# Kernel optimization log

Measured on AMD Instinct MI355X. Metric: run time of the kernel, lower is better.

The kernel has to match this reference:

```python
import jax, jax.numpy as jnp
import numpy as np

BN_EPS = 1e-5


def setup_inputs() -> dict:
    key = jax.random.key(0)
    ks = jax.random.split(key, 16)
    N, E, D, H = 100000, 1200000, 64, 128
    return {
        "x": jax.random.normal(ks[0], (N, D), dtype=jnp.float32),
        "edge_index": jax.random.randint(ks[1], (2, E), 0, N, dtype=jnp.int64),
        "edge_weight": jax.random.uniform(ks[2], (E,), dtype=jnp.float32),
        "edge_features": jax.random.normal(ks[3], (E, 16), dtype=jnp.float32),
        "adj": jnp.zeros((1,), dtype=jnp.float32),
        "T": 1,
        "bn_gamma": jax.random.uniform(ks[4], (D,), dtype=jnp.float32) + 0.5,
        "bn_beta": jax.random.normal(ks[5], (D,), dtype=jnp.float32) * 0.1,
        "W_l": jax.random.normal(ks[6], (D, H), dtype=jnp.float32) / np.sqrt(D),
        "b_l": jax.random.normal(ks[7], (H,), dtype=jnp.float32) * 0.01,
        "W_r": jax.random.normal(ks[8], (D, H), dtype=jnp.float32) / np.sqrt(D),
        "W1": jax.random.normal(ks[9], (H, 16), dtype=jnp.float32) / np.sqrt(H),
        "b1": jax.random.normal(ks[10], (16,), dtype=jnp.float32) * 0.01,
        "W2": jax.random.normal(ks[11], (16, 2), dtype=jnp.float32) / 4.0,
        "b2": jax.random.normal(ks[12], (2,), dtype=jnp.float32) * 0.01,
    }


def reference(x, edge_index, edge_weight, edge_features, adj, T,
              bn_gamma, bn_beta, W_l, b_l, W_r, W1, b1, W2, b2):
    # edge_weight, edge_features, adj, T are accepted but unused, matching the
    # original module's forward.
    N = x.shape[0]
    # BatchNorm1d (training mode: batch statistics, biased variance)
    mean = jnp.mean(x, axis=0)
    var = jnp.var(x, axis=0)
    xn = (x - mean) * jax.lax.rsqrt(var + BN_EPS) * bn_gamma + bn_beta

    # SAGEConv with mean aggregation: out = lin_l(mean_{j->i} x_j) + lin_r(x_i)
    src, dst = edge_index[0], edge_index[1]
    agg = jax.ops.segment_sum(xn[src], dst, num_segments=N)  # [N, D]
    deg = jax.ops.segment_sum(jnp.ones_like(dst, dtype=xn.dtype), dst,
                              num_segments=N)
    agg = agg / jnp.maximum(deg, 1.0)[:, None]
    h = agg @ W_l + b_l + xn @ W_r  # [N, H]
    h = jax.nn.relu(h)

    # classifier head: Linear(H,16) -> ReLU -> Linear(16,2)
    out = jax.nn.relu(h @ W1 + b1) @ W2 + b2  # [N, 2]
    return out
```

## Files before the change

### kernel.cpp

```cpp
#include <hip/hip_runtime.h>

#define FEAT 64
#define HDIM 128
#define BN_EPS 1e-5f

#define BSH 7
#define NB_MAX 1024
#define SCHUNK 4096
#define SEG 4096
#define CAP 2048

#define PSOFF 1280
#define PQOFF (PSOFF + 65536)
#define WCOFF (PQOFF + 65536)
#define XNOFF (WCOFF + 8192)

typedef __attribute__((ext_vector_type(8))) short bf16x8;
typedef __attribute__((ext_vector_type(4))) float f32x4;

#define GL16(gp, lp)                                                        \
    __builtin_amdgcn_global_load_lds(                                       \
        (const __attribute__((address_space(1))) unsigned int*)(gp),        \
        (__attribute__((address_space(3))) unsigned int*)(lp), 16, 0, 0)

__device__ inline unsigned short f2bf(float f) {
    union { float f; unsigned int u; } v;
    v.f = f;
    unsigned int r = (v.u + 0x7FFFu + ((v.u >> 16) & 1u)) >> 16;
    return (unsigned short)r;
}
__device__ inline float bf2f(unsigned short b) {
    union { unsigned int u; float f; } v;
    v.u = ((unsigned int)b) << 16;
    return v.f;
}

__global__ __launch_bounds__(256) void kA(const float* __restrict__ x,
                                          float* __restrict__ ws,
                                          const float* __restrict__ Wl,
                                          const float* __restrict__ Wr,
                                          unsigned short* __restrict__ Wc,
                                          const int* __restrict__ ei,
                                          int* __restrict__ bktCnt,
                                          int* __restrict__ pairs,
                                          int N, int E, int nb, int sbin) {
    __shared__ float4 sS[4][16];
    __shared__ float4 sQ[4][16];
    __shared__ int hist[NB_MAX];
    __shared__ int base[NB_MAX];
    int blk = blockIdx.x, t = threadIdx.x;
    if (blk < sbin) {
        int chunk = blk;
        int e0 = chunk * SCHUNK;
        int e1 = min(E, e0 + SCHUNK);
        for (int b = t; b < nb; b += 256) hist[b] = 0;
        __syncthreads();
        for (int e = e0 + t; e < e1; e += 256)
            atomicAdd(&hist[((unsigned)ei[E + e]) >> BSH], 1);
        __syncthreads();
        int rot = (chunk * 131) % nb;
        for (int j = t; j < nb; j += 256) {
            int b = j + rot;
            if (b >= nb) b -= nb;
            int c = hist[b];
            base[b] = c ? atomicAdd(&bktCnt[b], c) : 0;
            hist[b] = 0;
        }
        __syncthreads();
        for (int e = e0 + t; e < e1; e += 256) {
            int src = ei[e];
            int dst = ei[E + e];
            int b = ((unsigned)dst) >> BSH;
            int off = atomicAdd(&hist[b], 1);
            int pos = base[b] + off;
            if (pos < CAP) pairs[b * CAP + pos] = (src << BSH) | (dst & 127);
        }
    } else if (blk < sbin + 1024) {
        int sblk = blk - sbin;
        int rpb = (N + 1023) >> 10;
        int colg = t & 15, rowi = t >> 4;
        int lane = t & 63, wv = t >> 6;
        const float4* x4 = (const float4*)x;
        float4 s4 = {0.f, 0.f, 0.f, 0.f}, q4 = {0.f, 0.f, 0.f, 0.f};
        int r0 = sblk * rpb;
        for (int i = rowi; i < rpb; i += 16) {
            int r = r0 + i;
            if (r < N) {
                float4 v = x4[r * 16 + colg];
                s4.x += v.x; s4.y += v.y; s4.z += v.z; s4.w += v.w;
                q4.x += v.x * v.x; q4.y += v.y * v.y;
                q4.z += v.z * v.z; q4.w += v.w * v.w;
            }
        }
#pragma unroll
        for (int mk = 16; mk <= 32; mk <<= 1) {
            s4.x += __shfl_xor(s4.x, mk); s4.y += __shfl_xor(s4.y, mk);
            s4.z += __shfl_xor(s4.z, mk); s4.w += __shfl_xor(s4.w, mk);
            q4.x += __shfl_xor(q4.x, mk); q4.y += __shfl_xor(q4.y, mk);
            q4.z += __shfl_xor(q4.z, mk); q4.w += __shfl_xor(q4.w, mk);
        }
        if (lane < 16) { sS[wv][lane] = s4; sQ[wv][lane] = q4; }
        __syncthreads();
        if (t < 16) {
            float4 a = sS[0][t], b4 = sQ[0][t];
#pragma unroll
            for (int w = 1; w < 4; w++) {
                a.x += sS[w][t].x; a.y += sS[w][t].y;
                a.z += sS[w][t].z; a.w += sS[w][t].w;
                b4.x += sQ[w][t].x; b4.y += sQ[w][t].y;
                b4.z += sQ[w][t].z; b4.w += sQ[w][t].w;
            }
            int c0 = t * 4;
            ws[PSOFF + (c0 + 0) * 1024 + sblk] = a.x;
            ws[PSOFF + (c0 + 1) * 1024 + sblk] = a.y;
            ws[PSOFF + (c0 + 2) * 1024 + sblk] = a.z;
            ws[PSOFF + (c0 + 3) * 1024 + sblk] = a.w;
            ws[PQOFF + (c0 + 0) * 1024 + sblk] = b4.x;
            ws[PQOFF + (c0 + 1) * 1024 + sblk] = b4.y;
            ws[PQOFF + (c0 + 2) * 1024 + sblk] = b4.z;
            ws[PQOFF + (c0 + 3) * 1024 + sblk] = b4.w;
        }
    } else {
        int id = (blk - sbin - 1024) * 256 + t;
        int n = id >> 7, k = id & 127;
        float w = (k < 64) ? Wl[k * HDIM + n] : Wr[(k - 64) * HDIM + n];
        Wc[((k >> 5) * 128 + n) * 32 + (k & 31)] = f2bf(w);
    }
}

__global__ __launch_bounds__(256) void kB(float* __restrict__ ws,
                                          const float* __restrict__ gamma,
                                          const float* __restrict__ beta, int N) {
    __shared__ float r1[256], r2[256];
    int blk = blockIdx.x, t = threadIdx.x;
    const float* pS = ws + PSOFF + blk * 1024;
    const float* pQ = ws + PQOFF + blk * 1024;
    float s = 0.f, q = 0.f;
    for (int j = t; j < 1024; j += 256) { s += pS[j]; q += pQ[j]; }
    r1[t] = s;
    r2[t] = q;
    __syncthreads();
    for (int off = 128; off > 0; off >>= 1) {
        if (t < off) { r1[t] += r1[t + off]; r2[t] += r2[t + off]; }
        __syncthreads();
    }
    if (t == 0) {
        float invN = 1.0f / (float)N;
        float mean = r1[0] * invN;
        float var = r2[0] * invN - mean * mean;
        float sc = rsqrtf(var + BN_EPS) * gamma[blk];
        ws[128 + blk] = sc;
        ws[192 + blk] = beta[blk] - mean * sc;
    }
}

__global__ __launch_bounds__(256) void k3_norm(const float* __restrict__ x,
                                               const float* __restrict__ ws,
                                               unsigned short* __restrict__ xn, int N) {
    const float4* x4 = (const float4*)x;
    ushort4* o4 = (ushort4*)xn;
    int n4 = N * (FEAT / 4);
    int stride = gridDim.x * blockDim.x;
    for (int i = blockIdx.x * blockDim.x + threadIdx.x; i < n4; i += stride) {
        int cg = (i & 15) << 2;
        float4 v = x4[i];
        float4 sc = *(const float4*)(ws + 128 + cg);
        float4 sh = *(const float4*)(ws + 192 + cg);
        ushort4 o;
        o.x = f2bf(v.x * sc.x + sh.x);
        o.y = f2bf(v.y * sc.y + sh.y);
        o.z = f2bf(v.z * sc.z + sh.z);
        o.w = f2bf(v.w * sc.w + sh.w);
        o4[i] = o;
    }
}

__global__ __launch_bounds__(512) void kda(const int* __restrict__ pairs,
                                           const int* __restrict__ bktCnt,
                                           const unsigned short* __restrict__ xn,
                                           unsigned short* __restrict__ agg, int N) {
    __shared__ int sidx[SEG];
    __shared__ int cnt[128], nstart[128], ncur[128];
    int b = blockIdx.x;
    int base = b << BSH;
    int total = min(bktCnt[b], CAP);
    int bs = b * CAP, be = bs + total;
    int t = threadIdx.x;
    int lane = t & 63, wv = t >> 6;
    int part = lane & 7, slot = lane >> 3;

    if (total <= SEG) {
        if (t < 128) cnt[t] = 0;
        __syncthreads();
        for (int i = bs + t; i < be; i += 512)
            atomicAdd(&cnt[pairs[i] & 127], 1);
        __syncthreads();
        if (wv == 0) {
            int c0 = cnt[lane], c1 = cnt[64 + lane];
            int a = c0, d = c1;
#pragma unroll
            for (int off = 1; off < 64; off <<= 1) {
                int ta = __shfl_up(a, off);
                int td = __shfl_up(d, off);
                if (lane >= off) { a += ta; d += td; }
            }
            int totA = __shfl(a, 63);
            d += totA;
            nstart[lane] = a - c0;
            ncur[lane] = a - c0;
            nstart[64 + lane] = d - c1;
            ncur[64 + lane] = d - c1;
        }
        __syncthreads();
        for (int i = bs + t; i < be; i += 512) {
            int p = pairs[i];
            int nid = p & 127;
            int pos = atomicAdd(&ncur[nid], 1);
            sidx[pos] = (p >> BSH) << 6;
        }
        __syncthreads();

        int nA = wv * 16 + slot;
        int nB = nA + 8;
        int stA = nstart[nA], dA = cnt[nA];
        int stB = nstart[nB], dB = cnt[nB];
        float accA[8], accB[8];
#pragma unroll
        for (int j = 0; j < 8; j++) { accA[j] = 0.f; accB[j] = 0.f; }
        bf16x8 vA = {}, vB = {};
        for (int e = 0;; e++) {
            bool pA = e < dA, pB = e < dB;
            if (!__any(pA || pB)) break;
            if (pA) vA = *(const bf16x8*)(xn + sidx[stA + e] + part * 8);
            if (pB) vB = *(const bf16x8*)(xn + sidx[stB + e] + part * 8);
#pragma unroll
            for (int j = 0; j < 8; j++) {
                accA[j] += pA ? bf2f((unsigned short)vA[j]) : 0.f;
                accB[j] += pB ? bf2f((unsigned short)vB[j]) : 0.f;
            }
        }
        int nodeA = base + nA;
        int nodeB = base + nB;
        if (nodeA < N) {
            float dinv = (dA > 0) ? (1.0f / (float)dA) : 0.0f;
            union { bf16x8 v; unsigned short u[8]; } o;
#pragma unroll
            for (int j = 0; j < 8; j++) o.u[j] = f2bf(accA[j] * dinv);
            *(bf16x8*)(agg + (size_t)nodeA * FEAT + part * 8) = o.v;
        }
        if (nodeB < N) {
            float dinv = (dB > 0) ? (1.0f / (float)dB) : 0.0f;
            union { bf16x8 v; unsigned short u[8]; } o;
#pragma unroll
            for (int j = 0; j < 8; j++) o.u[j] = f2bf(accB[j] * dinv);
            *(bf16x8*)(agg + (size_t)nodeB * FEAT + part * 8) = o.v;
        }
    } else {
        for (int ni = wv; ni < 128; ni += 8) {
            int node = base + ni;
            if (node >= N) continue;
            float acc = 0.f;
            int deg = 0;
            for (int i = bs; i < be; i++) {
                int p = pairs[i];
                if ((p & 127) == ni) {
                    acc += bf2f(xn[((p >> BSH) << 6) + lane]);
                    deg++;
                }
            }
            float dinv = (deg > 0) ? (1.0f / (float)deg) : 0.0f;
            agg[(size_t)node * FEAT + lane] = f2bf(acc * dinv);
        }
    }
}

__global__ __launch_bounds__(256, 3) void k5_gemm(
    const unsigned short* __restrict__ agg, const unsigned short* __restrict__ xn,
    const unsigned short* __restrict__ Wc, const float* __restrict__ bl,
    const float* __restrict__ W1, const float* __restrict__ b1,
    const float* __restrict__ W2, const float* __restrict__ b2,
    float* __restrict__ out, int N) {
    __shared__ unsigned char tile[16384];
    __shared__ float hq[64][17];
    int t = threadIdx.x;
    int lane = t & 63;
    int wv = t >> 6;
    int rh = wv & 1;
    int ch = wv >> 1;
    int c = lane & 15;
    int q = lane >> 4;
    int row0 = blockIdx.x * 64;

    {
        int rrow = t >> 3;
        int sseg = t & 7;
#pragma unroll
        for (int r = 0; r < 2; r++) {
            int row = r * 32 + rrow;
            int grow = min(row0 + row, N - 1);
            int seg = sseg ^ (row & 7);
            unsigned ldso = (unsigned)(r * 4096 + wv * 1024);
            GL16(agg + (size_t)grow * 64 + seg * 8, &tile[ldso]);
            GL16(xn + (size_t)grow * 64 + seg * 8, &tile[8192 + ldso]);
        }
    }
    __syncthreads();

    f32x4 acc[2][4];
    f32x4 z = {0.f, 0.f, 0.f, 0.f};
#pragma unroll
    for (int rt = 0; rt < 2; rt++)
#pragma unroll
        for (int nt = 0; nt < 4; nt++) acc[rt][nt] = z;

#pragma unroll
    for (int kt = 0; kt < 4; kt++) {
        bf16x8 bfr[4];
#pragma unroll
        for (int nt = 0; nt < 4; nt++) {
            int col = ch * 64 + nt * 16 + c;
            bfr[nt] = *(const bf16x8*)(Wc + ((size_t)kt * 128 + col) * 32 + q * 8);
        }
        const unsigned char* abase = &tile[(kt < 2) ? 0 : 8192];
        int sg = (kt & 1) * 4 + q;
        bf16x8 af[2];
#pragma unroll
        for (int rt = 0; rt < 2; rt++) {
            int rowL = rh * 32 + rt * 16 + c;
            af[rt] = *(const bf16x8*)&abase[rowL * 128 + ((sg ^ (rowL & 7)) << 4)];
        }
#pragma unroll
        for (int rt = 0; rt < 2; rt++)
#pragma unroll
            for (int nt = 0; nt < 4; nt++)
                acc[rt][nt] = __builtin_amdgcn_mfma_f32_16x16x32_bf16(
                    af[rt], bfr[nt], acc[rt][nt], 0, 0, 0);
    }

    float bln[4];
    float4 w1v[4][4];
#pragma unroll
    for (int nt = 0; nt < 4; nt++) {
        int col = ch * 64 + nt * 16 + c;
        bln[nt] = bl[col];
        const float4* wp = (const float4*)(W1 + col * 16);
#pragma unroll
        for (int qq = 0; qq < 4; qq++) w1v[nt][qq] = wp[qq];
    }
    int m = ((c & 1) << 3) | ((c & 2) << 1) | ((c & 4) >> 1) | ((c & 8) >> 3);
    float b1v = b1[m];
    float w2x = W2[2 * m];
    float w2y = W2[2 * m + 1];

    float sv[2][4];
#pragma unroll
    for (int rt = 0; rt < 2; rt++) {
#pragma unroll
        for (int r = 0; r < 4; r++) {
            float tp[16];
#pragma unroll
            for (int j = 0; j < 16; j++) tp[j] = 0.f;
#pragma unroll
            for (int nt = 0; nt < 4; nt++) {
                float hv = fmaxf(acc[rt][nt][r] + bln[nt], 0.f);
#pragma unroll
                for (int qq = 0; qq < 4; qq++) {
                    tp[qq * 4 + 0] += hv * w1v[nt][qq].x;
                    tp[qq * 4 + 1] += hv * w1v[nt][qq].y;
                    tp[qq * 4 + 2] += hv * w1v[nt][qq].z;
                    tp[qq * 4 + 3] += hv * w1v[nt][qq].w;
                }
            }
            float u[8];
#pragma unroll
            for (int k = 0; k < 8; k++) {
                float keep = (c & 1) ? tp[k + 8] : tp[k];
                float send = (c & 1) ? tp[k] : tp[k + 8];
                u[k] = keep + __shfl_xor(send, 1);
            }
            float v4[4];
#pragma unroll
            for (int k = 0; k < 4; k++) {
                float keep = (c & 2) ? u[k + 4] : u[k];
                float send = (c & 2) ? u[k] : u[k + 4];
                v4[k] = keep + __shfl_xor(send, 2);
            }
            float w2v[2];
#pragma unroll
            for (int k = 0; k < 2; k++) {
                float keep = (c & 4) ? v4[k + 2] : v4[k];
                float send = (c & 4) ? v4[k] : v4[k + 2];
                w2v[k] = keep + __shfl_xor(send, 4);
            }
            {
                float keep = (c & 8) ? w2v[1] : w2v[0];
                float send = (c & 8) ? w2v[0] : w2v[1];
                sv[rt][r] = keep + __shfl_xor(send, 8);
            }
        }
    }

    if (ch == 0) {
#pragma unroll
        for (int rt = 0; rt < 2; rt++)
#pragma unroll
            for (int r = 0; r < 4; r++)
                hq[rh * 32 + rt * 16 + q * 4 + r][m] = sv[rt][r];
    }
    __syncthreads();
    if (ch == 1) {
        float b2x = b2[0], b2y = b2[1];
#pragma unroll
        for (int rt = 0; rt < 2; rt++) {
#pragma unroll
            for (int r = 0; r < 4; r++) {
                int row = rh * 32 + rt * 16 + q * 4 + r;
                float tm = sv[rt][r] + hq[row][m] + b1v;
                tm = fmaxf(tm, 0.f);
                float o0 = tm * w2x;
                float o1 = tm * w2y;
#pragma unroll
                for (int mk = 1; mk < 16; mk <<= 1) {
                    o0 += __shfl_xor(o0, mk);
                    o1 += __shfl_xor(o1, mk);
                }
                if (c == 0) {
                    int rowg = row0 + row;
                    if (rowg < N) {
                        out[(size_t)rowg * 2 + 0] = o0 + b2x;
                        out[(size_t)rowg * 2 + 1] = o1 + b2y;
                    }
                }
            }
        }
    }
}

extern "C" void kernel_launch(void* const* d_in, const int* in_sizes, int n_in,
                              void* d_out, int out_size, void* d_ws, size_t ws_size,
                              hipStream_t stream) {
    const float* x = (const float*)d_in[0];
    const int* ei = (const int*)d_in[1];
    const float* gamma = (const float*)d_in[6];
    const float* beta = (const float*)d_in[7];
    const float* Wl = (const float*)d_in[8];
    const float* bl = (const float*)d_in[9];
    const float* Wr = (const float*)d_in[10];
    const float* W1 = (const float*)d_in[11];
    const float* b1 = (const float*)d_in[12];
    const float* W2 = (const float*)d_in[13];
    const float* b2 = (const float*)d_in[14];

    int N = in_sizes[0] / FEAT;
    int E = in_sizes[1] / 2;
    int nb = (N + 127) >> BSH;
    int sbin = (E + SCHUNK - 1) / SCHUNK;

    float* ws = (float*)d_ws;
    int* wsi = (int*)d_ws;
    int bcOff = 256;
    int aggOff = XNOFF + N * 32;
    int pairsOff = aggOff + N * 32;

    unsigned short* xnp = (unsigned short*)(ws + XNOFF);
    unsigned short* aggp = (unsigned short*)(ws + aggOff);
    unsigned short* wcp = (unsigned short*)(ws + WCOFF);
    int* bktCnt = wsi + bcOff;
    int* pairs = wsi + pairsOff;

    float* out = (float*)d_out;

    hipMemsetAsync(bktCnt, 0, NB_MAX * sizeof(int), stream);
    hipLaunchKernelGGL(kA, dim3(sbin + 1088), dim3(256), 0, stream,
                       x, ws, Wl, Wr, wcp, ei, bktCnt, pairs, N, E, nb, sbin);
    hipLaunchKernelGGL(kB, dim3(64), dim3(256), 0, stream, ws, gamma, beta, N);
    hipLaunchKernelGGL(k3_norm, dim3(2048), dim3(256), 0, stream, x, ws, xnp, N);
    hipLaunchKernelGGL(kda, dim3(nb), dim3(512), 0, stream,
                       pairs, bktCnt, xnp, aggp, N);
    hipLaunchKernelGGL(k5_gemm, dim3((N + 63) / 64), dim3(256), 0, stream,
                       aggp, xnp, wcp, bl, W1, b1, W2, b2, out, N);
}
```

Measured before the change: 249.0 us.

## Replace global atomic bucket offsets with per-chunk histogram plus scan pass

Edge binning now writes a per-chunk bucket histogram to global memory. A scan in the BN-stats kernel turns it into deterministic per-chunk bucket offsets, and the pair scatter moves into the normalization kernel. This removes the global atomicAdd on bucket counters and the memset, and splits the scatter work across kernels so it can overlap with normalization. Chunk size is doubled and the oversized-bucket fallback in aggregation is dropped. It adds histogram/offset buffers and an extra read of the edge list.

```diff
diff --git a/kernel.cpp b/kernel.cpp
--- a/kernel.cpp
+++ b/kernel.cpp
@@ -6,8 +6,8 @@
 
 #define BSH 7
 #define NB_MAX 1024
-#define SCHUNK 4096
-#define SEG 4096
+#define SCHUNK 8192
+#define CST 256
 #define CAP 2048
 
 #define PSOFF 1280
@@ -41,40 +41,24 @@
                                           const float* __restrict__ Wr,
                                           unsigned short* __restrict__ Wc,
                                           const int* __restrict__ ei,
-                                          int* __restrict__ bktCnt,
-                                          int* __restrict__ pairs,
+                                          int* __restrict__ hg,
                                           int N, int E, int nb, int sbin) {
     __shared__ float4 sS[4][16];
     __shared__ float4 sQ[4][16];
     __shared__ int hist[NB_MAX];
-    __shared__ int base[NB_MAX];
     int blk = blockIdx.x, t = threadIdx.x;
     if (blk < sbin) {
-        int chunk = blk;
-        int e0 = chunk * SCHUNK;
-        int e1 = min(E, e0 + SCHUNK);
-        for (int b = t; b < nb; b += 256) hist[b] = 0;
+        int c = blk;
+        int e0 = c * SCHUNK;
+        for (int b = t; b < NB_MAX; b += 256) hist[b] = 0;
         __syncthreads();
-        for (int e = e0 + t; e < e1; e += 256)
-            atomicAdd(&hist[((unsigned)ei[E + e]) >> BSH], 1);
+#pragma unroll
+        for (int i = 0; i < SCHUNK / 256; i++) {
+            int e = e0 + i * 256 + t;
+            if (e < E) atomicAdd(&hist[((unsigned)ei[E + e]) >> BSH], 1);
+        }
         __syncthreads();
-        int rot = (chunk * 131) % nb;
-        for (int j = t; j < nb; j += 256) {
-            int b = j + rot;
-            if (b >= nb) b -= nb;
-            int c = hist[b];
-            base[b] = c ? atomicAdd(&bktCnt[b], c) : 0;
-            hist[b] = 0;
-        }
-        __syncthreads();
-        for (int e = e0 + t; e < e1; e += 256) {
-            int src = ei[e];
-            int dst = ei[E + e];
-            int b = ((unsigned)dst) >> BSH;
-            int off = atomicAdd(&hist[b], 1);
-            int pos = base[b] + off;
-            if (pos < CAP) pairs[b * CAP + pos] = (src << BSH) | (dst & 127);
-        }
+        for (int b = t; b < nb; b += 256) hg[b * CST + c] = hist[b];
     } else if (blk < sbin + 1024) {
         int sblk = blk - sbin;
         int rpb = (N + 1023) >> 10;
@@ -130,147 +114,182 @@
 
 __global__ __launch_bounds__(256) void kB(float* __restrict__ ws,
                                           const float* __restrict__ gamma,
-                                          const float* __restrict__ beta, int N) {
-    __shared__ float r1[256], r2[256];
+                                          const float* __restrict__ beta,
+                                          const int* __restrict__ hg,
+                                          int* __restrict__ cb,
+                                          int* __restrict__ bktTot,
+                                          int N, int nb, int sbin) {
     int blk = blockIdx.x, t = threadIdx.x;
-    const float* pS = ws + PSOFF + blk * 1024;
-    const float* pQ = ws + PQOFF + blk * 1024;
-    float s = 0.f, q = 0.f;
-    for (int j = t; j < 1024; j += 256) { s += pS[j]; q += pQ[j]; }
-    r1[t] = s;
-    r2[t] = q;
-    __syncthreads();
-    for (int off = 128; off > 0; off >>= 1) {
-        if (t < off) { r1[t] += r1[t + off]; r2[t] += r2[t + off]; }
+    if (blk < 64) {
+        __shared__ float r1[256], r2[256];
+        const float* pS = ws + PSOFF + blk * 1024;
+        const float* pQ = ws + PQOFF + blk * 1024;
+        float s = 0.f, q = 0.f;
+        for (int j = t; j < 1024; j += 256) { s += pS[j]; q += pQ[j]; }
+        r1[t] = s;
+        r2[t] = q;
         __syncthreads();
-    }
-    if (t == 0) {
-        float invN = 1.0f / (float)N;
-        float mean = r1[0] * invN;
-        float var = r2[0] * invN - mean * mean;
-        float sc = rsqrtf(var + BN_EPS) * gamma[blk];
-        ws[128 + blk] = sc;
-        ws[192 + blk] = beta[blk] - mean * sc;
+        for (int off = 128; off > 0; off >>= 1) {
+            if (t < off) { r1[t] += r1[t + off]; r2[t] += r2[t + off]; }
+            __syncthreads();
+        }
+        if (t == 0) {
+            float invN = 1.0f / (float)N;
+            float mean = r1[0] * invN;
+            float var = r2[0] * invN - mean * mean;
+            float sc = rsqrtf(var + BN_EPS) * gamma[blk];
+            ws[128 + blk] = sc;
+            ws[192 + blk] = beta[blk] - mean * sc;
+        }
+    } else {
+        int lane = t & 63, wv = t >> 6;
+        int b = (blk - 64) * 4 + wv;
+        if (b >= nb) return;
+        int running = 0;
+        for (int t0 = 0; t0 < sbin; t0 += 64) {
+            int c = t0 + lane;
+            int v = (c < sbin) ? hg[b * CST + c] : 0;
+            int incl = v;
+#pragma unroll
+            for (int off = 1; off < 64; off <<= 1) {
+                int tv = __shfl_up(incl, off);
+                if (lane >= off) incl += tv;
+            }
+            if (c < sbin) cb[b * CST + c] = running + incl - v;
+            running += __shfl(incl, 63);
+        }
+        if (lane == 0) bktTot[b] = running;
     }
 }
 
 __global__ __launch_bounds__(256) void k3_norm(const float* __restrict__ x,
                                                const float* __restrict__ ws,
-                                               unsigned short* __restrict__ xn, int N) {
-    const float4* x4 = (const float4*)x;
-    ushort4* o4 = (ushort4*)xn;
-    int n4 = N * (FEAT / 4);
-    int stride = gridDim.x * blockDim.x;
-    for (int i = blockIdx.x * blockDim.x + threadIdx.x; i < n4; i += stride) {
-        int cg = (i & 15) << 2;
-        float4 v = x4[i];
-        float4 sc = *(const float4*)(ws + 128 + cg);
-        float4 sh = *(const float4*)(ws + 192 + cg);
-        ushort4 o;
-        o.x = f2bf(v.x * sc.x + sh.x);
-        o.y = f2bf(v.y * sc.y + sh.y);
-        o.z = f2bf(v.z * sc.z + sh.z);
-        o.w = f2bf(v.w * sc.w + sh.w);
-        o4[i] = o;
+                                               unsigned short* __restrict__ xn,
+                                               const int* __restrict__ ei,
+                                               const int* __restrict__ cb,
+                                               int* __restrict__ pairs,
+                                               int N, int E, int nb, int sbin) {
+    __shared__ int lh[NB_MAX];
+    __shared__ int cbL[NB_MAX];
+    int blk = blockIdx.x, t = threadIdx.x;
+    if (blk < 2048) {
+        const float4* x4 = (const float4*)x;
+        ushort4* o4 = (ushort4*)xn;
+        int n4 = N * (FEAT / 4);
+        int stride = 2048 * 256;
+        for (int i = blk * 256 + t; i < n4; i += stride) {
+            int cg = (i & 15) << 2;
+            float4 v = x4[i];
+            float4 sc = *(const float4*)(ws + 128 + cg);
+            float4 sh = *(const float4*)(ws + 192 + cg);
+            ushort4 o;
+            o.x = f2bf(v.x * sc.x + sh.x);
+            o.y = f2bf(v.y * sc.y + sh.y);
+            o.z = f2bf(v.z * sc.z + sh.z);
+            o.w = f2bf(v.w * sc.w + sh.w);
+            o4[i] = o;
+        }
+    } else {
+        int c = blk - 2048;
+        int e0 = c * SCHUNK;
+        for (int b = t; b < nb; b += 256) {
+            lh[b] = 0;
+            cbL[b] = cb[b * CST + c];
+        }
+        __syncthreads();
+#pragma unroll
+        for (int i = 0; i < SCHUNK / 256; i++) {
+            int e = e0 + i * 256 + t;
+            if (e < E) {
+                int src = ei[e];
+                int dst = ei[E + e];
+                int b = ((unsigned)dst) >> BSH;
+                int off = atomicAdd(&lh[b], 1);
+                int rel = cbL[b] + off;
+                if (rel < CAP) pairs[b * CAP + rel] = (src << BSH) | (dst & 127);
+            }
+        }
     }
 }
 
 __global__ __launch_bounds__(512) void kda(const int* __restrict__ pairs,
-                                           const int* __restrict__ bktCnt,
+                                           const int* __restrict__ bktTot,
                                            const unsigned short* __restrict__ xn,
                                            unsigned short* __restrict__ agg, int N) {
-    __shared__ int sidx[SEG];
+    __shared__ int sidx[CAP];
     __shared__ int cnt[128], nstart[128], ncur[128];
     int b = blockIdx.x;
     int base = b << BSH;
-    int total = min(bktCnt[b], CAP);
+    int total = min(bktTot[b], CAP);
     int bs = b * CAP, be = bs + total;
     int t = threadIdx.x;
     int lane = t & 63, wv = t >> 6;
     int part = lane & 7, slot = lane >> 3;
 
-    if (total <= SEG) {
-        if (t < 128) cnt[t] = 0;
-        __syncthreads();
-        for (int i = bs + t; i < be; i += 512)
-            atomicAdd(&cnt[pairs[i] & 127], 1);
-        __syncthreads();
-        if (wv == 0) {
-            int c0 = cnt[lane], c1 = cnt[64 + lane];
-            int a = c0, d = c1;
-#pragma unroll
-            for (int off = 1; off < 64; off <<= 1) {
-                int ta = __shfl_up(a, off);
-                int td = __shfl_up(d, off);
-                if (lane >= off) { a += ta; d += td; }
-            }
-            int totA = __shfl(a, 63);
-            d += totA;
-            nstart[lane] = a - c0;
-            ncur[lane] = a - c0;
-            nstart[64 + lane] = d - c1;
-            ncur[64 + lane] = d - c1;
-        }
-        __syncthreads();
-        for (int i = bs + t; i < be; i += 512) {
-            int p = pairs[i];
-            int nid = p & 127;
-            int pos = atomicAdd(&ncur[nid], 1);
-            sidx[pos] = (p >> BSH) << 6;
-        }
-        __syncthreads();
-
-        int nA = wv * 16 + slot;
-        int nB = nA + 8;
-        int stA = nstart[nA], dA = cnt[nA];
-        int stB = nstart[nB], dB = cnt[nB];
-        float accA[8], accB[8];
-#pragma unroll
-        for (int j = 0; j < 8; j++) { accA[j] = 0.f; accB[j] = 0.f; }
-        bf16x8 vA = {}, vB = {};
-        for (int e = 0;; e++) {
-            bool pA = e < dA, pB = e < dB;
-            if (!__any(pA || pB)) break;
-            if (pA) vA = *(const bf16x8*)(xn + sidx[stA + e] + part * 8);
-            if (pB) vB = *(const bf16x8*)(xn + sidx[stB + e] + part * 8);
-#pragma unroll
-            for (int j = 0; j < 8; j++) {
-                accA[j] += pA ? bf2f((unsigned short)vA[j]) : 0.f;
-                accB[j] += pB ? bf2f((unsigned short)vB[j]) : 0.f;
-            }
-        }
-        int nodeA = base + nA;
-        int nodeB = base + nB;
-        if (nodeA < N) {
-            float dinv = (dA > 0) ? (1.0f / (float)dA) : 0.0f;
-            union { bf16x8 v; unsigned short u[8]; } o;
-#pragma unroll
-            for (int j = 0; j < 8; j++) o.u[j] = f2bf(accA[j] * dinv);
-            *(bf16x8*)(agg + (size_t)nodeA * FEAT + part * 8) = o.v;
-        }
-        if (nodeB < N) {
-            float dinv = (dB > 0) ? (1.0f / (float)dB) : 0.0f;
-            union { bf16x8 v; unsigned short u[8]; } o;
-#pragma unroll
-            for (int j = 0; j < 8; j++) o.u[j] = f2bf(accB[j] * dinv);
-            *(bf16x8*)(agg + (size_t)nodeB * FEAT + part * 8) = o.v;
-        }
-    } else {
-        for (int ni = wv; ni < 128; ni += 8) {
-            int node = base + ni;
-            if (node >= N) continue;
-            float acc = 0.f;
-            int deg = 0;
-            for (int i = bs; i < be; i++) {
-                int p = pairs[i];
-                if ((p & 127) == ni) {
-                    acc += bf2f(xn[((p >> BSH) << 6) + lane]);
-                    deg++;
-                }
-            }
-            float dinv = (deg > 0) ? (1.0f / (float)deg) : 0.0f;
-            agg[(size_t)node * FEAT + lane] = f2bf(acc * dinv);
-        }
+    if (t < 128) cnt[t] = 0;
+    __syncthreads();
+    for (int i = bs + t; i < be; i += 512)
+        atomicAdd(&cnt[pairs[i] & 127], 1);
+    __syncthreads();
+    if (wv == 0) {
+        int c0 = cnt[lane], c1 = cnt[64 + lane];
+        int a = c0, d = c1;
+#pragma unroll
+        for (int off = 1; off < 64; off <<= 1) {
+            int ta = __shfl_up(a, off);
+            int td = __shfl_up(d, off);
+            if (lane >= off) { a += ta; d += td; }
+        }
+        int totA = __shfl(a, 63);
+        d += totA;
+        nstart[lane] = a - c0;
+        ncur[lane] = a - c0;
+        nstart[64 + lane] = d - c1;
+        ncur[64 + lane] = d - c1;
+    }
+    __syncthreads();
+    for (int i = bs + t; i < be; i += 512) {
+        int p = pairs[i];
+        int nid = p & 127;
+        int pos = atomicAdd(&ncur[nid], 1);
+        sidx[pos] = (p >> BSH) << 6;
+    }
+    __syncthreads();
+
+    int nA = wv * 16 + slot;
+    int nB = nA + 8;
+    int stA = nstart[nA], dA = cnt[nA];
+    int stB = nstart[nB], dB = cnt[nB];
+    float accA[8], accB[8];
+#pragma unroll
+    for (int j = 0; j < 8; j++) { accA[j] = 0.f; accB[j] = 0.f; }
+    bf16x8 vA = {}, vB = {};
+    for (int e = 0;; e++) {
+        bool pA = e < dA, pB = e < dB;
+        if (!__any(pA || pB)) break;
+        if (pA) vA = *(const bf16x8*)(xn + sidx[stA + e] + part * 8);
+        if (pB) vB = *(const bf16x8*)(xn + sidx[stB + e] + part * 8);
+#pragma unroll
+        for (int j = 0; j < 8; j++) {
+            accA[j] += pA ? bf2f((unsigned short)vA[j]) : 0.f;
+            accB[j] += pB ? bf2f((unsigned short)vB[j]) : 0.f;
+        }
+    }
+    int nodeA = base + nA;
+    int nodeB = base + nB;
+    if (nodeA < N) {
+        float dinv = (dA > 0) ? (1.0f / (float)dA) : 0.0f;
+        union { bf16x8 v; unsigned short u[8]; } o;
+#pragma unroll
+        for (int j = 0; j < 8; j++) o.u[j] = f2bf(accA[j] * dinv);
+        *(bf16x8*)(agg + (size_t)nodeA * FEAT + part * 8) = o.v;
+    }
+    if (nodeB < N) {
+        float dinv = (dB > 0) ? (1.0f / (float)dB) : 0.0f;
+        union { bf16x8 v; unsigned short u[8]; } o;
+#pragma unroll
+        for (int j = 0; j < 8; j++) o.u[j] = f2bf(accB[j] * dinv);
+        *(bf16x8*)(agg + (size_t)nodeB * FEAT + part * 8) = o.v;
     }
 }
 
@@ -455,28 +474,34 @@
     int E = in_sizes[1] / 2;
     int nb = (N + 127) >> BSH;
     int sbin = (E + SCHUNK - 1) / SCHUNK;
+    int nsb = (nb + 3) / 4;
 
     float* ws = (float*)d_ws;
     int* wsi = (int*)d_ws;
-    int bcOff = 256;
     int aggOff = XNOFF + N * 32;
-    int pairsOff = aggOff + N * 32;
+    int hgOff = aggOff + N * 32;
+    int cbOff = hgOff + NB_MAX * CST;
+    int btOff = cbOff + NB_MAX * CST;
+    int pairsOff = (btOff + NB_MAX + 63) & ~63;
 
     unsigned short* xnp = (unsigned short*)(ws + XNOFF);
     unsigned short* aggp = (unsigned short*)(ws + aggOff);
     unsigned short* wcp = (unsigned short*)(ws + WCOFF);
-    int* bktCnt = wsi + bcOff;
+    int* hg = wsi + hgOff;
+    int* cb = wsi + cbOff;
+    int* bktTot = wsi + btOff;
     int* pairs = wsi + pairsOff;
 
     float* out = (float*)d_out;
 
-    hipMemsetAsync(bktCnt, 0, NB_MAX * sizeof(int), stream);
     hipLaunchKernelGGL(kA, dim3(sbin + 1088), dim3(256), 0, stream,
-                       x, ws, Wl, Wr, wcp, ei, bktCnt, pairs, N, E, nb, sbin);
-    hipLaunchKernelGGL(kB, dim3(64), dim3(256), 0, stream, ws, gamma, beta, N);
-    hipLaunchKernelGGL(k3_norm, dim3(2048), dim3(256), 0, stream, x, ws, xnp, N);
+                       x, ws, Wl, Wr, wcp, ei, hg, N, E, nb, sbin);
+    hipLaunchKernelGGL(kB, dim3(64 + nsb), dim3(256), 0, stream,
+                       ws, gamma, beta, hg, cb, bktTot, N, nb, sbin);
+    hipLaunchKernelGGL(k3_norm, dim3(2048 + sbin), dim3(256), 0, stream,
+                       x, ws, xnp, ei, cb, pairs, N, E, nb, sbin);
     hipLaunchKernelGGL(kda, dim3(nb), dim3(512), 0, stream,
-                       pairs, bktCnt, xnp, aggp, N);
+                       pairs, bktTot, xnp, aggp, N);
     hipLaunchKernelGGL(k5_gemm, dim3((N + 63) / 64), dim3(256), 0, stream,
                        aggp, xnp, wcp, bl, W1, b1, W2, b2, out, N);
 }
```

After: 265.5 us. +6.7%, slower.
